# Kernel tuning notes

Measured on AMD Instinct MI355X. Metric: run time of the kernel, lower is better.

## Reference

```python
import jax, jax.numpy as jnp
import numpy as np

DT = 0.1
LN_EPS = 1e-5
B, T, D_IN, H, N_APP = 128, 2048, 16, 256, 10


def layer_norm(x, g, b):
    mu = jnp.mean(x, axis=-1, keepdims=True)
    var = jnp.mean(jnp.square(x - mu), axis=-1, keepdims=True)
    return (x - mu) * jax.lax.rsqrt(var + LN_EPS) * g + b


def setup_inputs() -> dict:
    key = jax.random.key(0)
    ks = jax.random.split(key, 4)
    x = jax.random.normal(ks[0], (B, T, D_IN), dtype=jnp.float32)
    W_in = jax.random.normal(ks[1], (H, D_IN), dtype=jnp.float32) * (1.0 / np.sqrt(D_IN))
    b_in = jnp.zeros((H,), dtype=jnp.float32)
    tau_param = jnp.ones((H,), dtype=jnp.float32)
    # xavier_uniform for (H, H)
    limit = np.sqrt(6.0 / (H + H))
    W_rec = jax.random.uniform(ks[2], (H, H), dtype=jnp.float32, minval=-limit, maxval=limit)
    g_intra = jnp.ones((H,), dtype=jnp.float32)
    b_intra = jnp.zeros((H,), dtype=jnp.float32)
    g_norm = jnp.ones((H,), dtype=jnp.float32)
    b_norm = jnp.zeros((H,), dtype=jnp.float32)
    W_head = jax.random.normal(ks[3], (H, N_APP), dtype=jnp.float32) * (1.0 / np.sqrt(H))
    b_head = jnp.zeros((N_APP,), dtype=jnp.float32)
    return dict(x=x, W_in=W_in, b_in=b_in, tau_param=tau_param, W_rec=W_rec,
                g_intra=g_intra, b_intra=b_intra, g_norm=g_norm, b_norm=b_norm,
                W_head=W_head, b_head=b_head)


def reference(x, W_in, b_in, tau_param, W_rec, g_intra, b_intra, g_norm, b_norm, W_head, b_head):
    # x: (B, T, D_IN)
    tau = jax.nn.softplus(tau_param)  # (H,), fixed
    # Precompute input projection for all timesteps: (B, T, H)
    inp_proj = jnp.einsum('bti,hi->bth', x, W_in) + b_in
    xs = jnp.swapaxes(inp_proj, 0, 1)  # (T, B, H) for scan

    def step(h, u_t):
        rec = h @ W_rec                       # (B, H)
        f_t = jnp.tanh(layer_norm(u_t + rec, g_intra, b_intra))
        dh = (-h / tau + f_t) * DT
        h_new = jnp.clip(h + dh, -10.0, 10.0)
        return h_new, None

    h0 = jnp.zeros((x.shape[0], W_rec.shape[0]), dtype=x.dtype)
    h, _ = jax.lax.scan(step, h0, xs)
    h = layer_norm(h, g_norm, b_norm)
    return h @ W_head + b_head  # (B, N_APP)
```

## Files before the change

### kernel.cpp

```cpp
#include <hip/hip_runtime.h>


#define BB     128
#define TT     2048
#define DIN    16
#define HH     256
#define NAPP   10
#define NT     256
#define DT_STEP 0.1f
#define LN_EPS_C 1e-5f

typedef _Float16 half2_t __attribute__((ext_vector_type(2)));

template<int CTRL>
__device__ __forceinline__ float dpp_mov0(float x) {
    return __builtin_bit_cast(float,
        __builtin_amdgcn_update_dpp(0, __builtin_bit_cast(int, x), CTRL, 0xF, 0xF, true));
}

__device__ __forceinline__ void wave_reduce2(float& s1, float& s2) {
    s1 += dpp_mov0<0x111>(s1); s2 += dpp_mov0<0x111>(s2);
    s1 += dpp_mov0<0x112>(s1); s2 += dpp_mov0<0x112>(s2);
    s1 += dpp_mov0<0x114>(s1); s2 += dpp_mov0<0x114>(s2);
    s1 += dpp_mov0<0x118>(s1); s2 += dpp_mov0<0x118>(s2);
    s1 += dpp_mov0<0x142>(s1); s2 += dpp_mov0<0x142>(s2);
    s1 += dpp_mov0<0x143>(s1); s2 += dpp_mov0<0x143>(s2);
}

__device__ __forceinline__ half2_t as_h2(int v) { return __builtin_bit_cast(half2_t, v); }
__device__ __forceinline__ float rl63(float v) {
    return __builtin_bit_cast(float,
        __builtin_amdgcn_readlane(__builtin_bit_cast(int, v), 63));
}
__device__ __forceinline__ float softplus_f(float v) {
    return (v > 20.f) ? v : log1pf(__expf(v));
}

__global__ __launch_bounds__(NT, 1)
void liquid_scan_kernel(const float* __restrict__ x,
                        const float* __restrict__ W_in,
                        const float* __restrict__ b_in,
                        const float* __restrict__ tau_param,
                        const float* __restrict__ W_rec,
                        const float* __restrict__ g_intra,
                        const float* __restrict__ b_intra,
                        const float* __restrict__ g_norm,
                        const float* __restrict__ b_norm,
                        const float* __restrict__ W_head,
                        const float* __restrict__ b_head,
                        float* __restrict__ out)
{
    const int tid  = threadIdx.x;
    const int b    = blockIdx.x;
    const int lane = tid & 63;
    const int kq   = tid >> 6;
    const int j0   = lane * 4;

    __shared__ __align__(16) float        x_lds[TT * DIN];
    __shared__ __align__(16) float        part[4][HH];
    __shared__ __align__(16) unsigned int hpk_lds[HH / 2];

    {
        const float4* xg = (const float4*)(x + (size_t)b * TT * DIN);
        float4* xl = (float4*)x_lds;
        #pragma unroll 4
        for (int i = tid; i < TT * DIN / 4; i += NT) xl[i] = xg[i];
    }
    if (tid < HH / 2) hpk_lds[tid] = 0u;

    half2_t w2[4][32];
    #pragma unroll
    for (int p = 0; p < 32; ++p) {
        const float* r0 = W_rec + (size_t)(64 * kq + 2 * p) * HH + j0;
        const float* r1 = r0 + HH;
        #pragma unroll
        for (int c = 0; c < 4; ++c) {
            half2_t t2; t2.x = (_Float16)r0[c]; t2.y = (_Float16)r1[c];
            w2[c][p] = t2;
        }
    }

    float win[4][4];
    #pragma unroll
    for (int c = 0; c < 4; ++c) {
        #pragma unroll
        for (int r = 0; r < 4; ++r)
            win[c][r] = W_in[(size_t)(j0 + c) * DIN + 4 * kq + r];
    }

    float bi_[4], gi_[4], bbi_[4], itau_[4], gn_[4], bn_[4];
    float hj[4] = {0.f, 0.f, 0.f, 0.f};
    if (kq == 0) {
        const float4 v0 = *(const float4*)(b_in      + j0);
        const float4 v1 = *(const float4*)(g_intra   + j0);
        const float4 v2 = *(const float4*)(b_intra   + j0);
        const float4 v3 = *(const float4*)(tau_param + j0);
        const float4 v4 = *(const float4*)(g_norm    + j0);
        const float4 v5 = *(const float4*)(b_norm    + j0);
        bi_[0] = v0.x; bi_[1] = v0.y; bi_[2] = v0.z; bi_[3] = v0.w;
        gi_[0] = v1.x; gi_[1] = v1.y; gi_[2] = v1.z; gi_[3] = v1.w;
        bbi_[0] = v2.x; bbi_[1] = v2.y; bbi_[2] = v2.z; bbi_[3] = v2.w;
        itau_[0] = 1.f / softplus_f(v3.x); itau_[1] = 1.f / softplus_f(v3.y);
        itau_[2] = 1.f / softplus_f(v3.z); itau_[3] = 1.f / softplus_f(v3.w);
        gn_[0] = v4.x; gn_[1] = v4.y; gn_[2] = v4.z; gn_[3] = v4.w;
        bn_[0] = v5.x; bn_[1] = v5.y; bn_[2] = v5.z; bn_[3] = v5.w;
    }
    __syncthreads();

    for (int t = 0; t < TT; ++t) {
        const float4 xs = *(const float4*)&x_lds[t * DIN + 4 * kq];
        const int hpk = (int)hpk_lds[kq * 32 + (lane & 31)];

        float a0 = 0.f, a1 = 0.f, a2 = 0.f, a3 = 0.f;
        #pragma unroll
        for (int p = 0; p < 32; ++p) {
            const int r = __builtin_amdgcn_readlane(hpk, p);
            a0 = __builtin_amdgcn_fdot2(as_h2(r), w2[0][p], a0, false);
            a1 = __builtin_amdgcn_fdot2(as_h2(r), w2[1][p], a1, false);
            a2 = __builtin_amdgcn_fdot2(as_h2(r), w2[2][p], a2, false);
            a3 = __builtin_amdgcn_fdot2(as_h2(r), w2[3][p], a3, false);
        }
        a0 = fmaf(xs.x, win[0][0], a0); a0 = fmaf(xs.y, win[0][1], a0);
        a0 = fmaf(xs.z, win[0][2], a0); a0 = fmaf(xs.w, win[0][3], a0);
        a1 = fmaf(xs.x, win[1][0], a1); a1 = fmaf(xs.y, win[1][1], a1);
        a1 = fmaf(xs.z, win[1][2], a1); a1 = fmaf(xs.w, win[1][3], a1);
        a2 = fmaf(xs.x, win[2][0], a2); a2 = fmaf(xs.y, win[2][1], a2);
        a2 = fmaf(xs.z, win[2][2], a2); a2 = fmaf(xs.w, win[2][3], a2);
        a3 = fmaf(xs.x, win[3][0], a3); a3 = fmaf(xs.y, win[3][1], a3);
        a3 = fmaf(xs.z, win[3][2], a3); a3 = fmaf(xs.w, win[3][3], a3);

        if (kq) ((float4*)part[kq])[lane] = make_float4(a0, a1, a2, a3);
        __syncthreads();

        if (kq == 0) {
            const float4 p1 = ((const float4*)part[1])[lane];
            const float4 p2 = ((const float4*)part[2])[lane];
            const float4 p3 = ((const float4*)part[3])[lane];
            float u[4];
            u[0] = a0 + (p1.x + p2.x) + (p3.x + bi_[0]);
            u[1] = a1 + (p1.y + p2.y) + (p3.y + bi_[1]);
            u[2] = a2 + (p1.z + p2.z) + (p3.z + bi_[2]);
            u[3] = a3 + (p1.w + p2.w) + (p3.w + bi_[3]);
            float s1 = (u[0] + u[1]) + (u[2] + u[3]);
            float s2 = (u[0] * u[0] + u[1] * u[1]) + (u[2] * u[2] + u[3] * u[3]);
            wave_reduce2(s1, s2);
            const float S1 = rl63(s1);
            const float S2 = rl63(s2);
            const float mu  = S1 * (1.f / HH);
            const float var = S2 * (1.f / HH) - mu * mu;
            const float rs  = rsqrtf(var + LN_EPS_C);
            #pragma unroll
            for (int c = 0; c < 4; ++c) {
                const float xn = (u[c] - mu) * rs * gi_[c] + bbi_[c];
                const float e = __expf(2.f * xn);
                const float f = 1.f - 2.f / (e + 1.f);
                float v = hj[c] + (f - hj[c] * itau_[c]) * DT_STEP;
                v = fminf(10.f, fmaxf(-10.f, v));
                hj[c] = v;
            }
            uint2 pk;
            pk.x = __builtin_bit_cast(unsigned int, __builtin_amdgcn_cvt_pkrtz(hj[0], hj[1]));
            pk.y = __builtin_bit_cast(unsigned int, __builtin_amdgcn_cvt_pkrtz(hj[2], hj[3]));
            ((uint2*)hpk_lds)[lane] = pk;
        }
        __syncthreads();
    }

    if (kq == 0) {
        float s1 = (hj[0] + hj[1]) + (hj[2] + hj[3]);
        float s2 = (hj[0] * hj[0] + hj[1] * hj[1]) + (hj[2] * hj[2] + hj[3] * hj[3]);
        wave_reduce2(s1, s2);
        const float S1 = rl63(s1);
        const float S2 = rl63(s2);
        const float mu  = S1 * (1.f / HH);
        const float var = S2 * (1.f / HH) - mu * mu;
        const float rs  = rsqrtf(var + LN_EPS_C);
        float4 ho;
        ho.x = (hj[0] - mu) * rs * gn_[0] + bn_[0];
        ho.y = (hj[1] - mu) * rs * gn_[1] + bn_[1];
        ho.z = (hj[2] - mu) * rs * gn_[2] + bn_[2];
        ho.w = (hj[3] - mu) * rs * gn_[3] + bn_[3];
        ((float4*)part[0])[lane] = ho;
    }
    __syncthreads();
    if (tid < NAPP) {
        float o = b_head[tid];
        for (int jj = 0; jj < HH; ++jj)
            o = fmaf(part[0][jj], W_head[jj * NAPP + tid], o);
        out[(size_t)b * NAPP + tid] = o;
    }
}

extern "C" void kernel_launch(void* const* d_in, const int* in_sizes, int n_in,
                              void* d_out, int out_size, void* d_ws, size_t ws_size,
                              hipStream_t stream) {
    const float* x       = (const float*)d_in[0];
    const float* W_in    = (const float*)d_in[1];
    const float* b_in    = (const float*)d_in[2];
    const float* tau     = (const float*)d_in[3];
    const float* W_rec   = (const float*)d_in[4];
    const float* g_intra = (const float*)d_in[5];
    const float* b_intra = (const float*)d_in[6];
    const float* g_norm  = (const float*)d_in[7];
    const float* b_norm  = (const float*)d_in[8];
    const float* W_head  = (const float*)d_in[9];
    const float* b_head  = (const float*)d_in[10];
    float* out = (float*)d_out;

    hipLaunchKernelGGL(liquid_scan_kernel, dim3(BB), dim3(NT), 0, stream,
                       x, W_in, b_in, tau, W_rec, g_intra, b_intra,
                       g_norm, b_norm, W_head, b_head, out);
}
```

Before: 1.711 ms.

## Replicate LayerNorm/state update across waves to drop a barrier per step

Every wave now reads all four partial sums and redundantly computes the LayerNorm, tanh and state update, so each wave holds the packed half-precision hidden state in registers. Because no wave has to wait for a single finisher, one of the two per-step barriers is removed, and a double-buffered partial array makes the single remaining barrier enough. Hardware rcp and rsq builtins replace the precise divide and rsqrt. The trade is that four waves repeat the same elementwise work and the DPP reductions, and the approximate reciprocal may shift numerics slightly.

```diff
diff --git a/kernel.cpp b/kernel.cpp
--- a/kernel.cpp
+++ b/kernel.cpp
@@ -56,9 +56,8 @@
     const int kq   = tid >> 6;
     const int j0   = lane * 4;
 
-    __shared__ __align__(16) float        x_lds[TT * DIN];
-    __shared__ __align__(16) float        part[4][HH];
-    __shared__ __align__(16) unsigned int hpk_lds[HH / 2];
+    __shared__ __align__(16) float x_lds[TT * DIN];
+    __shared__ __align__(16) float part[2][4][HH];
 
     {
         const float4* xg = (const float4*)(x + (size_t)b * TT * DIN);
@@ -66,7 +65,6 @@
         #pragma unroll 4
         for (int i = tid; i < TT * DIN / 4; i += NT) xl[i] = xg[i];
     }
-    if (tid < HH / 2) hpk_lds[tid] = 0u;
 
     half2_t w2[4][32];
     #pragma unroll
@@ -89,8 +87,7 @@
     }
 
     float bi_[4], gi_[4], bbi_[4], itau_[4], gn_[4], bn_[4];
-    float hj[4] = {0.f, 0.f, 0.f, 0.f};
-    if (kq == 0) {
+    {
         const float4 v0 = *(const float4*)(b_in      + j0);
         const float4 v1 = *(const float4*)(g_intra   + j0);
         const float4 v2 = *(const float4*)(b_intra   + j0);
@@ -105,16 +102,23 @@
         gn_[0] = v4.x; gn_[1] = v4.y; gn_[2] = v4.z; gn_[3] = v4.w;
         bn_[0] = v5.x; bn_[1] = v5.y; bn_[2] = v5.z; bn_[3] = v5.w;
     }
+
+    float hj[4] = {0.f, 0.f, 0.f, 0.f};
+    int pkX = 0, pkY = 0;
+    const int rlbase = 16 * kq;
+    const int o1 = (kq + 1) & 3, o2 = (kq + 2) & 3, o3 = (kq + 3) & 3;
+
     __syncthreads();
 
+    #pragma unroll 1
     for (int t = 0; t < TT; ++t) {
         const float4 xs = *(const float4*)&x_lds[t * DIN + 4 * kq];
-        const int hpk = (int)hpk_lds[kq * 32 + (lane & 31)];
 
         float a0 = 0.f, a1 = 0.f, a2 = 0.f, a3 = 0.f;
         #pragma unroll
         for (int p = 0; p < 32; ++p) {
-            const int r = __builtin_amdgcn_readlane(hpk, p);
+            const int r = __builtin_amdgcn_readlane((p & 1) ? pkY : pkX,
+                                                    rlbase + (p >> 1));
             a0 = __builtin_amdgcn_fdot2(as_h2(r), w2[0][p], a0, false);
             a1 = __builtin_amdgcn_fdot2(as_h2(r), w2[1][p], a1, false);
             a2 = __builtin_amdgcn_fdot2(as_h2(r), w2[2][p], a2, false);
@@ -129,41 +133,37 @@
         a3 = fmaf(xs.x, win[3][0], a3); a3 = fmaf(xs.y, win[3][1], a3);
         a3 = fmaf(xs.z, win[3][2], a3); a3 = fmaf(xs.w, win[3][3], a3);
 
-        if (kq) ((float4*)part[kq])[lane] = make_float4(a0, a1, a2, a3);
+        ((float4*)part[t & 1][kq])[lane] = make_float4(a0, a1, a2, a3);
         __syncthreads();
 
-        if (kq == 0) {
-            const float4 p1 = ((const float4*)part[1])[lane];
-            const float4 p2 = ((const float4*)part[2])[lane];
-            const float4 p3 = ((const float4*)part[3])[lane];
-            float u[4];
-            u[0] = a0 + (p1.x + p2.x) + (p3.x + bi_[0]);
-            u[1] = a1 + (p1.y + p2.y) + (p3.y + bi_[1]);
-            u[2] = a2 + (p1.z + p2.z) + (p3.z + bi_[2]);
-            u[3] = a3 + (p1.w + p2.w) + (p3.w + bi_[3]);
-            float s1 = (u[0] + u[1]) + (u[2] + u[3]);
-            float s2 = (u[0] * u[0] + u[1] * u[1]) + (u[2] * u[2] + u[3] * u[3]);
-            wave_reduce2(s1, s2);
-            const float S1 = rl63(s1);
-            const float S2 = rl63(s2);
-            const float mu  = S1 * (1.f / HH);
-            const float var = S2 * (1.f / HH) - mu * mu;
-            const float rs  = rsqrtf(var + LN_EPS_C);
-            #pragma unroll
-            for (int c = 0; c < 4; ++c) {
-                const float xn = (u[c] - mu) * rs * gi_[c] + bbi_[c];
-                const float e = __expf(2.f * xn);
-                const float f = 1.f - 2.f / (e + 1.f);
-                float v = hj[c] + (f - hj[c] * itau_[c]) * DT_STEP;
-                v = fminf(10.f, fmaxf(-10.f, v));
-                hj[c] = v;
-            }
-            uint2 pk;
-            pk.x = __builtin_bit_cast(unsigned int, __builtin_amdgcn_cvt_pkrtz(hj[0], hj[1]));
-            pk.y = __builtin_bit_cast(unsigned int, __builtin_amdgcn_cvt_pkrtz(hj[2], hj[3]));
-            ((uint2*)hpk_lds)[lane] = pk;
+        const float4 p1 = ((const float4*)part[t & 1][o1])[lane];
+        const float4 p2 = ((const float4*)part[t & 1][o2])[lane];
+        const float4 p3 = ((const float4*)part[t & 1][o3])[lane];
+        float u[4];
+        u[0] = (a0 + p1.x) + (p2.x + p3.x) + bi_[0];
+        u[1] = (a1 + p1.y) + (p2.y + p3.y) + bi_[1];
+        u[2] = (a2 + p1.z) + (p2.z + p3.z) + bi_[2];
+        u[3] = (a3 + p1.w) + (p2.w + p3.w) + bi_[3];
+
+        float s1 = (u[0] + u[1]) + (u[2] + u[3]);
+        float s2 = (u[0] * u[0] + u[1] * u[1]) + (u[2] * u[2] + u[3] * u[3]);
+        wave_reduce2(s1, s2);
+        const float S1 = rl63(s1);
+        const float S2 = rl63(s2);
+        const float mu  = S1 * (1.f / HH);
+        const float var = S2 * (1.f / HH) - mu * mu;
+        const float rs  = __builtin_amdgcn_rsqf(var + LN_EPS_C);
+        #pragma unroll
+        for (int c = 0; c < 4; ++c) {
+            const float xn = (u[c] - mu) * rs * gi_[c] + bbi_[c];
+            const float e = __expf(2.f * xn);
+            const float f = 1.f - 2.f * __builtin_amdgcn_rcpf(e + 1.f);
+            float v = hj[c] + (f - hj[c] * itau_[c]) * DT_STEP;
+            v = fminf(10.f, fmaxf(-10.f, v));
+            hj[c] = v;
         }
-        __syncthreads();
+        pkX = __builtin_bit_cast(int, __builtin_amdgcn_cvt_pkrtz(hj[0], hj[1]));
+        pkY = __builtin_bit_cast(int, __builtin_amdgcn_cvt_pkrtz(hj[2], hj[3]));
     }
 
     if (kq == 0) {
@@ -180,13 +180,13 @@
         ho.y = (hj[1] - mu) * rs * gn_[1] + bn_[1];
         ho.z = (hj[2] - mu) * rs * gn_[2] + bn_[2];
         ho.w = (hj[3] - mu) * rs * gn_[3] + bn_[3];
-        ((float4*)part[0])[lane] = ho;
+        ((float4*)part[0][0])[lane] = ho;
     }
     __syncthreads();
     if (tid < NAPP) {
         float o = b_head[tid];
         for (int jj = 0; jj < HH; ++jj)
-            o = fmaf(part[0][jj], W_head[jj * NAPP + tid], o);
+            o = fmaf(part[0][0][jj], W_head[jj * NAPP + tid], o);
         out[(size_t)b * NAPP + tid] = o;
     }
 }
```

Result: slower. 1.756 ms (+2.6%).
